# Kernel optimization log

Measured on AMD Instinct MI355X. Metric: run time of the kernel, lower is better.

Reference implementation:

```python
import jax, jax.numpy as jnp
import numpy as np

# dims: B = clips*frames, L = x spatial tokens, C = input/output/linear_out dim,
# D = conv_dim_in, NV = conv_dim_out == linear_in (visual tokens), T = num_tk
B, L, C, D, NV, T, FR = 160, 196, 768, 512, 196, 87, 10
DM, DS = C // 2, C // 16          # affine bottleneck d_model, adapter down size
ALPHA, BETA, GAMMA = 0.3, 0.05, 0.05
EPS = 1e-5


def _ln(x, g, b):
    m = x.mean(-1, keepdims=True)
    v = jnp.mean((x - m) ** 2, axis=-1, keepdims=True)
    return (x - m) * jax.lax.rsqrt(v + EPS) * g + b


def _forward(x, vis_token, conv_w, conv_b, fc_w, fc_b, my_tokens, gate_av,
             a1_w, a1_b, v1_w, v1_b, bt_w, bt_b, vc_w, vc_b, v2_w, v2_b,
             a2_w, a2_b, vs_w, vs_b, tg_w, tg_b, lnb_g, lnb_b, down_w,
             bn1_g, bn1_b, bn1_m, bn1_v, up_w, bn2_g, bn2_b, bn2_m, bn2_v,
             lnp_g, lnp_b, gate):
    vt = vis_token[..., 0]                                   # (B,NV,D)
    # conv_adapter: 1x1 conv over channel axis D -> NV, then fc over token axis NV -> C
    h = jnp.einsum('od,bnd->bon', conv_w, vt) + conv_b[None, :, None]   # (B,NV,NV)
    V = jnp.einsum('bon,cn->boc', h, fc_w) + fc_b            # (B,NV,C)  == vis_token tokens

    # token <-> visual cross-attention
    rep = jnp.broadcast_to(my_tokens, (x.shape[0], T, C))    # (B,T,C)
    att_v2tk = jax.nn.softmax(jnp.einsum('btd,bnd->btn', rep, V), axis=-1)
    rep = rep + jnp.einsum('btn,bnd->btd', att_v2tk, V)

    xt = jnp.transpose(x[..., 0], (0, 2, 1))                 # (B,L,C)
    att_tk2x = jax.nn.softmax(jnp.einsum('bld,btd->blt', xt, rep), axis=-1)
    xt = xt + gate_av * jnp.einsum('blt,btd->bld', att_tk2x, rep)

    # channel attention
    audio = V.mean(axis=1)                                   # (B,C)
    aq1 = jax.nn.relu(audio @ a1_w.T + a1_b)[:, None, :]     # (B,1,C)
    vq1 = jax.nn.relu(xt @ v1_w.T + v1_b)                    # (B,L,C)
    avq = jax.nn.relu((aq1 * vq1).mean(axis=1) @ bt_w.T + bt_b)          # (B,DM)
    ch = jax.nn.sigmoid(avq @ vc_w.T + vc_b)[:, None, :]     # (B,1,C)
    cfeat = xt * (ch + 1.0)                                  # (B,L,C)

    # spatial attention
    cq = jax.nn.relu(cfeat @ v2_w.T + v2_b)                  # (B,L,DM)
    aq2 = jax.nn.relu(audio @ a2_w.T + a2_b)[:, None, :]     # (B,1,DM)
    s_tmp = (cq * aq2) @ vs_w.T + vs_b                       # (B,L,1)
    s_sig = jax.nn.sigmoid(s_tmp)                            # (B,L,1)
    spatial = jax.nn.softmax(jnp.tanh(s_tmp).transpose(0, 2, 1), axis=-1)  # (B,1,L)

    # temporal gate over frames
    audio_r = audio.reshape(B // FR, FR, C)
    temporal = jax.nn.sigmoid(audio_r @ tg_w.T + tg_b)[..., None]          # (bs,FR,1,1)

    x5 = xt.reshape(B // FR, FR, L, C)
    factor = (ALPHA * ch.reshape(B // FR, FR, 1, C)
              + BETA * s_sig.reshape(B // FR, FR, L, 1)
              + GAMMA * temporal + (1.0 - ALPHA))
    x6 = (x5 * factor).reshape(B, L, C)

    # bottleneck adapter: LN -> down(1x1) -> BN -> ReLU -> up(1x1) -> BN -> LN -> gate
    x6 = _ln(x6, lnb_g, lnb_b)
    z = jnp.einsum('blc,oc->blo', x6, down_w)                # (B,L,DS)
    z = (z - bn1_m) * jax.lax.rsqrt(bn1_v + EPS) * bn1_g + bn1_b
    z = jax.nn.relu(z)
    o = jnp.einsum('blo,co->blc', z, up_w)                   # (B,L,C)
    o = (o - bn2_m) * jax.lax.rsqrt(bn2_v + EPS) * bn2_g + bn2_b
    o = _ln(o, lnp_g, lnp_b)
    out = (gate * o).transpose(0, 2, 1)[..., None]           # (B,C,L,1)
    return out, spatial, temporal


def setup_inputs() -> dict:
    key = jax.random.key(0)
    ks = iter(jax.random.split(key, 48))
    nrm = lambda shp, s=0.02: jax.random.normal(next(ks), shp, jnp.float32) * s
    d = {}
    d['x'] = jax.random.normal(next(ks), (B, C, L, 1), jnp.float32)
    d['vis_token'] = jax.random.normal(next(ks), (B, NV, D, 1), jnp.float32)
    d['conv_w'] = nrm((NV, D)); d['conv_b'] = jnp.zeros((NV,), jnp.float32)
    d['fc_w'] = nrm((C, NV)); d['fc_b'] = jnp.zeros((C,), jnp.float32)
    d['my_tokens'] = jax.random.uniform(next(ks), (T, C), jnp.float32)
    d['gate_av'] = jnp.float32(0.5)
    d['a1_w'] = nrm((C, C)); d['a1_b'] = jnp.zeros((C,), jnp.float32)
    d['v1_w'] = nrm((C, C)); d['v1_b'] = jnp.zeros((C,), jnp.float32)
    d['bt_w'] = nrm((DM, C)); d['bt_b'] = jnp.zeros((DM,), jnp.float32)
    d['vc_w'] = nrm((C, DM)); d['vc_b'] = jnp.zeros((C,), jnp.float32)
    d['v2_w'] = nrm((DM, C)); d['v2_b'] = jnp.zeros((DM,), jnp.float32)
    d['a2_w'] = nrm((DM, C)); d['a2_b'] = jnp.zeros((DM,), jnp.float32)
    d['vs_w'] = nrm((1, DM)); d['vs_b'] = jnp.zeros((1,), jnp.float32)
    d['tg_w'] = nrm((1, C)); d['tg_b'] = jnp.zeros((1,), jnp.float32)
    d['lnb_g'] = jnp.ones((C,), jnp.float32); d['lnb_b'] = jnp.zeros((C,), jnp.float32)
    d['down_w'] = nrm((DS, C))
    d['bn1_g'] = jnp.ones((DS,), jnp.float32); d['bn1_b'] = jnp.zeros((DS,), jnp.float32)
    d['bn1_m'] = jnp.zeros((DS,), jnp.float32); d['bn1_v'] = jnp.ones((DS,), jnp.float32)
    d['up_w'] = nrm((C, DS))
    d['bn2_g'] = jnp.ones((C,), jnp.float32); d['bn2_b'] = jnp.zeros((C,), jnp.float32)
    d['bn2_m'] = jnp.zeros((C,), jnp.float32); d['bn2_v'] = jnp.ones((C,), jnp.float32)
    d['lnp_g'] = jnp.ones((C,), jnp.float32); d['lnp_b'] = jnp.zeros((C,), jnp.float32)
    d['gate'] = jnp.float32(1.0)
    return d


def reference(x, vis_token, conv_w, conv_b, fc_w, fc_b, my_tokens, gate_av,
              a1_w, a1_b, v1_w, v1_b, bt_w, bt_b, vc_w, vc_b, v2_w, v2_b,
              a2_w, a2_b, vs_w, vs_b, tg_w, tg_b, lnb_g, lnb_b, down_w,
              bn1_g, bn1_b, bn1_m, bn1_v, up_w, bn2_g, bn2_b, bn2_m, bn2_v,
              lnp_g, lnp_b, gate):
    return _forward(x, vis_token, conv_w, conv_b, fc_w, fc_b, my_tokens, gate_av,
                    a1_w, a1_b, v1_w, v1_b, bt_w, bt_b, vc_w, vc_b, v2_w, v2_b,
                    a2_w, a2_b, vs_w, vs_b, tg_w, tg_b, lnb_g, lnb_b, down_w,
                    bn1_g, bn1_b, bn1_m, bn1_v, up_w, bn2_g, bn2_b, bn2_m, bn2_v,
                    lnp_g, lnp_b, gate)
```

## Files before the change

### kernel.cpp

```cpp
#include <hip/hip_runtime.h>
#include <math.h>

#define Bc   160
#define Lc   196
#define Cc   768
#define Dc   512
#define NVc  196
#define Tc   87
#define FRc  10
#define DMc  384
#define DSc  48
#define LROW 196
#define ALPHAc 0.3f
#define BETAc  0.05f
#define GAMMAc 0.05f
#define EPSc   1e-5f

typedef __attribute__((ext_vector_type(8))) short short8v;
typedef __attribute__((ext_vector_type(4))) short short4v;
typedef __attribute__((ext_vector_type(4))) float f32x4;

__device__ __forceinline__ short f2bf(float f) {
    unsigned u = __builtin_bit_cast(unsigned, f);
    u = (u + 0x7FFFu + ((u >> 16) & 1u)) >> 16;
    return (short)u;
}
__device__ __forceinline__ float bf2f(short s) {
    unsigned u = ((unsigned)(unsigned short)s) << 16;
    return __builtin_bit_cast(float, u);
}

__device__ __forceinline__ void gload16(const void* g, void* l) {
    using GP = const __attribute__((address_space(1))) unsigned int*;
    using LP = __attribute__((address_space(3))) unsigned int*;
    __builtin_amdgcn_global_load_lds((GP)(uintptr_t)g, (LP)(uintptr_t)l, 16, 0, 0);
}

template<int BIAS, int ACT, int OUT, int STORE, int ADDT,
         bool ASCALE, bool RSUM, bool CSCALE, bool MULP, int BMODE, bool SWZ, bool FLAT,
         bool TSTORE>
__global__ __launch_bounds__(256) void mgemm(
    const short* __restrict__ A, long sA,
    const void* __restrict__ Bp, long sB, int ldB, int Klim,
    float* __restrict__ Cf, long sCf,
    short* __restrict__ Cb, long sCb, int ldC,
    float* __restrict__ Rf, long sRf,
    const void* __restrict__ Addp, long sAdd,
    const float* __restrict__ scalePtr,
    const float* __restrict__ biasR, const float* __restrict__ biasC,
    const float* __restrict__ ascale, const float* __restrict__ wcol,
    const float* __restrict__ csc, const float* __restrict__ mulp,
    int M, int N, int K, int nI, int nJ, float outScale)
{
    constexpr bool DEEP = (BMODE == 0) && !ASCALE;
    constexpr int LDSN = DEEP ? 24576 : 16384;
    constexpr int BOFF = DEEP ? 12288 : 8192;
    __shared__ short smem[LDSN];
    int b, iT, jT;
    if (FLAT) {
        b = 0;
        int id = blockIdx.x;
        int nI8 = (nI >> 3) << 3;
        int main_ = nI8 * nJ;
        if (id < main_) { int xx = id & 7; int q = id >> 3; jT = q % nJ; iT = (q / nJ) * 8 + xx; }
        else { int id2 = id - main_; iT = nI8 + id2 / nJ; jT = id2 % nJ; }
    } else {
        const int tiles = nI * nJ;
        int t;
        if (SWZ) { int id = blockIdx.x; b = ((id >> 3) / tiles) * 8 + (id & 7); t = (id >> 3) % tiles; }
        else     { int id = blockIdx.x; b = id / tiles; t = id % tiles; }
        iT = t / nJ; jT = t % nJ;
    }
    const int i0 = iT * 128, j0 = jT * 128;
    const int tid = threadIdx.x;
    const int wl = tid & 63, w = tid >> 6;
    const int wr = (w >> 1) * 64, wc = (w & 1) * 64;
    const int lr = wl & 15;
    const int kgl = (((wl >> 4) ^ (lr & 3) ^ ((lr >> 2) & 3)) * 8);
    const int sl8 = (((tid & 3) ^ ((tid >> 2) & 3) ^ ((tid >> 4) & 3)) * 8);
    const int grow = w * 16 + (wl >> 2);
    const int srow = tid >> 2;
    const short* Ab = A + (FLAT ? 0L : (long)b * sA);

    f32x4 acc[4][4] = {};

    auto STAGE = [&](short* Asb, short* Bsb, int k0) {
        if (!ASCALE) {
            #pragma unroll
            for (int h = 0; h < 2; ++h) {
                int gi = i0 + h * 64 + grow; if (gi > M - 1) gi = M - 1;
                gload16(Ab + (long)gi * K + k0 + sl8, Asb + h * 2048 + w * 512);
            }
        } else {
            #pragma unroll
            for (int h = 0; h < 2; ++h) {
                int r = srow + h * 64;
                int gi = i0 + r; if (gi > M - 1) gi = M - 1;
                short8v av = *(const short8v*)(Ab + (long)gi * K + k0 + (tid & 3) * 8);
                int bb = FLAT ? (gi / LROW) : b;
                const float* asb = ascale + (long)bb * K + k0 + (tid & 3) * 8;
                #pragma unroll
                for (int e = 0; e < 8; ++e) av[e] = f2bf(bf2f(av[e]) * asb[e]);
                *(short8v*)&Asb[r * 32 + sl8] = av;
            }
        }
        if (BMODE == 0) {
            const short* Bb = (const short*)Bp + (FLAT ? 0L : (long)b * sB);
            #pragma unroll
            for (int h = 0; h < 2; ++h) {
                int gj = j0 + h * 64 + grow; if (gj > N - 1) gj = N - 1;
                gload16(Bb + (long)gj * K + k0 + sl8, Bsb + h * 2048 + w * 512);
            }
        } else if (BMODE == 2) {
            const float* Bb = (const float*)Bp + (long)b * sB;
            #pragma unroll
            for (int h = 0; h < 2; ++h) {
                int r = srow + h * 64;
                int gj = j0 + r;
                short8v bv = {};
                if (gj < N) {
                    const float* p = Bb + (long)gj * K + k0 + (tid & 3) * 8;
                    float4 lo = *(const float4*)p, hi = *(const float4*)(p + 4);
                    bv[0] = f2bf(lo.x); bv[1] = f2bf(lo.y); bv[2] = f2bf(lo.z); bv[3] = f2bf(lo.w);
                    bv[4] = f2bf(hi.x); bv[5] = f2bf(hi.y); bv[6] = f2bf(hi.z); bv[7] = f2bf(hi.w);
                }
                *(short8v*)&Bsb[r * 32 + sl8] = bv;
            }
        } else if (BMODE == 1) {
            const short* Bb = (const short*)Bp + (long)b * sB;
            #pragma unroll
            for (int h = 0; h < 2; ++h) {
                int idx = tid + h * 256;
                int kk = idx >> 4, jg = idx & 15;
                int gk = k0 + kk, gj = j0 + jg * 8;
                short8v bv = {};
                if (gk < Klim && gj < N)
                    bv = *(const short8v*)(Bb + (long)gk * ldB + gj);
                #pragma unroll
                for (int e = 0; e < 8; ++e) {
                    int row = jg * 8 + e;
                    int slot = (kk >> 3) ^ (row & 3) ^ ((row >> 2) & 3);
                    Bsb[row * 32 + slot * 8 + (kk & 7)] = bv[e];
                }
            }
        }
    };

    auto COMPUTE = [&](const short* as, const short* bs) {
        short8v af[4], bfv[4];
        #pragma unroll
        for (int m = 0; m < 4; ++m) af[m]  = *(const short8v*)&as[(wr + m * 16 + lr) * 32 + kgl];
        #pragma unroll
        for (int n = 0; n < 4; ++n) bfv[n] = *(const short8v*)&bs[(wc + n * 16 + lr) * 32 + kgl];
        #pragma unroll
        for (int m = 0; m < 4; ++m)
            #pragma unroll
            for (int n = 0; n < 4; ++n)
                acc[m][n] = __builtin_amdgcn_mfma_f32_16x16x32_bf16(af[m], bfv[n], acc[m][n], 0, 0, 0);
    };

    const int nt = K >> 5;
    if (DEEP) {
        STAGE(smem, smem + BOFF, 0);
        if (nt > 1) STAGE(smem + 4096, smem + BOFF + 4096, 32);
        for (int tt = 0; tt < nt; ++tt) {
            if (tt + 1 < nt) asm volatile("s_waitcnt vmcnt(4)" ::: "memory");
            else             asm volatile("s_waitcnt vmcnt(0)" ::: "memory");
            __builtin_amdgcn_s_barrier();
            __builtin_amdgcn_sched_barrier(0);
            if (tt + 2 < nt) {
                int nb = (tt + 2) % 3;
                STAGE(smem + nb * 4096, smem + BOFF + nb * 4096, (tt + 2) * 32);
            }
            int cb = tt % 3;
            COMPUTE(smem + cb * 4096, smem + BOFF + cb * 4096);
        }
    } else {
        STAGE(smem, smem + BOFF, 0);
        for (int tt = 0; tt < nt; ++tt) {
            __syncthreads();
            if (tt + 1 < nt) {
                int nb = (tt + 1) & 1;
                STAGE(smem + nb * 4096, smem + BOFF + nb * 4096, (tt + 1) * 32);
            }
            int cb = tt & 1;
            COMPUTE(smem + cb * 4096, smem + BOFF + cb * 4096);
        }
    }

    const int colbase = j0 + wc;
    const int rowbase = i0 + wr;
    float scale = 1.f;
    if (ADDT) scale = scalePtr ? scalePtr[0] : 1.f;
    const int bA = FLAT ? (i0 / LROW) : 0;
    const bool straddle = FLAT && (((i0 + 127) / LROW) != bA);

    if (OUT == 0 && TSTORE) {
        float rsum[4] = {0.f, 0.f, 0.f, 0.f};
        float rsum2[4] = {0.f, 0.f, 0.f, 0.f};
        __syncthreads();
        #pragma unroll
        for (int n = 0; n < 4; ++n) {
            int col = wc + n * 16 + lr;
            int j = j0 + col;
            int jc = j < N ? j : N - 1;
            #pragma unroll
            for (int m = 0; m < 4; ++m) {
                #pragma unroll
                for (int r = 0; r < 4; ++r) {
                    int row = wr + m * 16 + (wl >> 4) * 4 + r;
                    int i = i0 + row;
                    int ic = i < M ? i : M - 1;
                    float v = acc[m][n][r];
                    if (BIAS == 1) v += biasR[ic];
                    else if (BIAS == 2) v += biasC[jc];
                    else if (BIAS == 3) v = v * biasR[jc] + biasC[jc];
                    if (ACT == 1) v = fmaxf(v, 0.f);
                    else if (ACT == 2) v = 1.f / (1.f + expf(-v));
                    else if (ACT == 3) v = 1.f + 1.f / (1.f + expf(-v));
                    if (CSCALE) v *= csc[jc];
                    if (MULP) v *= mulp[(long)ic * N + jc];
                    smem[row * 128 + col] = f2bf(v);
                    if (RSUM && j < N && i < M) {
                        if (FLAT && (i / LROW) != bA) rsum2[n] += v;
                        else rsum[n] += v;
                    }
                }
            }
        }
        if (RSUM) {
            #pragma unroll
            for (int n = 0; n < 4; ++n) {
                int j = colbase + n * 16 + lr;
                float s = rsum[n];
                s += __shfl_xor(s, 16, 64);
                s += __shfl_xor(s, 32, 64);
                float s2 = 0.f;
                if (FLAT && straddle) {
                    s2 = rsum2[n];
                    s2 += __shfl_xor(s2, 16, 64);
                    s2 += __shfl_xor(s2, 32, 64);
                }
                if ((wl >> 4) == 0 && j < N) {
                    atomicAdd(&Rf[(long)bA * sRf + (FLAT ? 0 : (long)b * sRf) + j], s * outScale);
                    if (FLAT && straddle)
                        atomicAdd(&Rf[(long)(bA + 1) * sRf + j], s2 * outScale);
                }
            }
        }
        __syncthreads();
        #pragma unroll
        for (int p = 0; p < 8; ++p) {
            int row = (tid >> 4) + p * 16;
            int i = i0 + row;
            int c8 = (tid & 15) * 8;
            int j = j0 + c8;
            if (i < M && j < ldC) {
                short8v sv = *(const short8v*)&smem[row * 128 + c8];
                if (ADDT == 2) {
                    const short* ap = (const short*)Addp + (long)b * sAdd + (long)i * N + j;
                    short8v av = *(const short8v*)ap;
                    #pragma unroll
                    for (int e = 0; e < 8; ++e) sv[e] = f2bf(bf2f(av[e]) + scale * bf2f(sv[e]));
                } else if (ADDT == 1) {
                    const float* ap = (const float*)Addp + (long)b * sAdd + (long)i * N + j;
                    f32x4 lo = *(const f32x4*)ap, hi = *(const f32x4*)(ap + 4);
                    #pragma unroll
                    for (int e = 0; e < 4; ++e) sv[e] = f2bf(lo[e] + scale * bf2f(sv[e]));
                    #pragma unroll
                    for (int e = 0; e < 4; ++e) sv[e + 4] = f2bf(hi[e] + scale * bf2f(sv[e + 4]));
                }
                *(short8v*)&Cb[(long)b * sCb + (long)i * ldC + j] = sv;
            }
        }
    } else if (OUT == 0) {
        float rsum[4] = {0.f, 0.f, 0.f, 0.f};
        float rsum2[4] = {0.f, 0.f, 0.f, 0.f};
        #pragma unroll
        for (int n = 0; n < 4; ++n) {
            int j = colbase + n * 16 + lr;
            if (j >= N) continue;
            #pragma unroll
            for (int m = 0; m < 4; ++m) {
                #pragma unroll
                for (int r = 0; r < 4; ++r) {
                    int i = rowbase + m * 16 + (wl >> 4) * 4 + r;
                    if (i >= M) continue;
                    float v = acc[m][n][r];
                    if (BIAS == 1) v += biasR[i];
                    else if (BIAS == 2) v += biasC[j];
                    else if (BIAS == 3) v = v * biasR[j] + biasC[j];
                    if (ACT == 1) v = fmaxf(v, 0.f);
                    else if (ACT == 2) v = 1.f / (1.f + expf(-v));
                    else if (ACT == 3) v = 1.f + 1.f / (1.f + expf(-v));
                    if (CSCALE) v *= csc[j];
                    if (MULP) v *= mulp[(long)i * N + j];
                    if (ADDT == 1) v = ((const float*)Addp)[(long)b * sAdd + (long)i * N + j] + scale * v;
                    else if (ADDT == 2) v = bf2f(((const short*)Addp)[(long)b * sAdd + (long)i * N + j]) + scale * v;
                    if (STORE & 1) Cf[(long)b * sCf + (long)i * N + j] = v;
                    if (STORE & 2) Cb[(long)b * sCb + (long)i * ldC + j] = f2bf(v);
                    if (RSUM) {
                        if (FLAT && (i / LROW) != bA) rsum2[n] += v;
                        else rsum[n] += v;
                    }
                }
            }
        }
        if (RSUM) {
            #pragma unroll
            for (int n = 0; n < 4; ++n) {
                int j = colbase + n * 16 + lr;
                float s = rsum[n];
                s += __shfl_xor(s, 16, 64);
                s += __shfl_xor(s, 32, 64);
                float s2 = 0.f;
                if (FLAT && straddle) {
                    s2 = rsum2[n];
                    s2 += __shfl_xor(s2, 16, 64);
                    s2 += __shfl_xor(s2, 32, 64);
                }
                if ((wl >> 4) == 0 && j < N) {
                    atomicAdd(&Rf[(long)bA * sRf + (FLAT ? 0 : (long)b * sRf) + j], s * outScale);
                    if (FLAT && straddle)
                        atomicAdd(&Rf[(long)(bA + 1) * sRf + j], s2 * outScale);
                }
            }
        }
    } else if (OUT == 1) {
        #pragma unroll
        for (int n = 0; n < 4; ++n) {
            int j = colbase + n * 16 + lr;
            if (j < N) {
                float s = 0.f, s2 = 0.f;
                #pragma unroll
                for (int m = 0; m < 4; ++m)
                    #pragma unroll
                    for (int r = 0; r < 4; ++r) {
                        int i = rowbase + m * 16 + (wl >> 4) * 4 + r;
                        if (i >= M) continue;
                        float v = acc[m][n][r];
                        if (BIAS == 2) v += biasC[j];
                        if (ACT == 1) v = fmaxf(v, 0.f);
                        if (FLAT && (i / LROW) != bA) s2 += v; else s += v;
                    }
                s += __shfl_xor(s, 16, 64);
                s += __shfl_xor(s, 32, 64);
                if (FLAT && straddle) {
                    s2 += __shfl_xor(s2, 16, 64);
                    s2 += __shfl_xor(s2, 32, 64);
                }
                if ((wl >> 4) == 0) {
                    atomicAdd(&Cf[(long)(FLAT ? bA : b) * sCf + j], s * outScale);
                    if (FLAT && straddle)
                        atomicAdd(&Cf[(long)(bA + 1) * sCf + j], s2 * outScale);
                }
            }
        }
    } else {
        #pragma unroll
        for (int m = 0; m < 4; ++m) {
            #pragma unroll
            for (int r = 0; r < 4; ++r) {
                int i = rowbase + m * 16 + (wl >> 4) * 4 + r;
                int bw = FLAT ? (i < M ? i / LROW : 0) : b;
                float s = 0.f;
                #pragma unroll
                for (int n = 0; n < 4; ++n) {
                    int j = colbase + n * 16 + lr;
                    if (j >= N) continue;
                    float v = acc[m][n][r];
                    if (BIAS == 2) v += biasC[j];
                    if (ACT == 1) v = fmaxf(v, 0.f);
                    s += v * wcol[(long)bw * N + j];
                }
                s += __shfl_xor(s, 1, 64);
                s += __shfl_xor(s, 2, 64);
                s += __shfl_xor(s, 4, 64);
                s += __shfl_xor(s, 8, 64);
                if (lr == 0 && i < M)
                    atomicAdd(&Cf[(FLAT ? (long)i : (long)b * sCf + i)], s * outScale);
            }
        }
    }
}

__global__ void k_cvt_weights(
    const float* __restrict__ my_tok, const float* __restrict__ conv_w,
    const float* __restrict__ a1_w, const float* __restrict__ v1_w,
    const float* __restrict__ bt_w, const float* __restrict__ vc_w,
    const float* __restrict__ v2_w, const float* __restrict__ a2_w,
    const float* __restrict__ down_w, const float* __restrict__ fc_w,
    const float* __restrict__ up_w,
    short* __restrict__ mytok_bf, short* __restrict__ wconv,
    short* __restrict__ wa1, short* __restrict__ wv1,
    short* __restrict__ wbt, short* __restrict__ wvc,
    short* __restrict__ wv2, short* __restrict__ wa2,
    short* __restrict__ wdown, short* __restrict__ wfc, short* __restrict__ wup)
{
    long idx = (long)blockIdx.x * 256 + threadIdx.x;
    if (idx < 66816)  { mytok_bf[idx] = f2bf(my_tok[idx]); return; }  idx -= 66816;
    if (idx < 100352) { wconv[idx] = f2bf(conv_w[idx]); return; }     idx -= 100352;
    if (idx < 589824) { wa1[idx] = f2bf(a1_w[idx]); return; }         idx -= 589824;
    if (idx < 589824) { wv1[idx] = f2bf(v1_w[idx]); return; }         idx -= 589824;
    if (idx < 294912) { wbt[idx] = f2bf(bt_w[idx]); return; }         idx -= 294912;
    if (idx < 294912) { wvc[idx] = f2bf(vc_w[idx]); return; }         idx -= 294912;
    if (idx < 294912) { wv2[idx] = f2bf(v2_w[idx]); return; }         idx -= 294912;
    if (idx < 294912) { wa2[idx] = f2bf(a2_w[idx]); return; }         idx -= 294912;
    if (idx < 36864)  { wdown[idx] = f2bf(down_w[idx]); return; }     idx -= 36864;
    if (idx < 172032) { int r = (int)(idx / 224), c = (int)(idx % 224);
                        wfc[idx] = (c < 196) ? f2bf(fc_w[(long)r * 196 + c]) : (short)0; return; }
    idx -= 172032;
    if (idx < 49152)  { int r = (int)(idx / 64), c = (int)(idx % 64);
                        wup[idx] = (c < 48) ? f2bf(up_w[(long)r * 48 + c]) : (short)0; }
}

__global__ void k_prep(const float* g1, const float* b1, const float* m1, const float* v1,
                       const float* g2, const float* b2, const float* m2, const float* v2,
                       float* scl1, float* sft1, float* scl2, float* sft2)
{
    int j = threadIdx.x;
    if (j < DSc) { float r = rsqrtf(v1[j] + EPSc) * g1[j]; scl1[j] = r; sft1[j] = b1[j] - m1[j] * r; }
    if (j < Cc)  { float r = rsqrtf(v2[j] + EPSc) * g2[j]; scl2[j] = r; sft2[j] = b2[j] - m2[j] * r; }
}

__global__ __launch_bounds__(256) void k_transpose(const float* __restrict__ x, short* __restrict__ xtb)
{
    __shared__ float tile[64][33];
    int b = blockIdx.z;
    int c0 = blockIdx.y * 64, l0 = blockIdx.x * 32;
    int tx = threadIdx.x & 31, ty = threadIdx.x >> 5;
    #pragma unroll
    for (int k = 0; k < 8; ++k) {
        int c = c0 + ty + 8 * k, l = l0 + tx;
        tile[ty + 8 * k][tx] = (l < Lc) ? x[((long)b * Cc + c) * Lc + l] : 0.f;
    }
    __syncthreads();
    int cg = threadIdx.x & 15, lw = threadIdx.x >> 4;
    #pragma unroll
    for (int p = 0; p < 2; ++p) {
        int l = l0 + lw + p * 16;
        if (l >= Lc) continue;
        int c = c0 + cg * 4;
        short4v sv;
        #pragma unroll
        for (int e = 0; e < 4; ++e) sv[e] = f2bf(tile[cg * 4 + e][lw + p * 16]);
        *(short4v*)(xtb + ((long)b * Lc + l) * Cc + c) = sv;
    }
}

__global__ __launch_bounds__(256) void k_audio_fin(
    const float* __restrict__ audio, short* __restrict__ audio_bf,
    const float* __restrict__ tg_w, const float* __restrict__ tg_b,
    float* __restrict__ tempv, float* __restrict__ outTemp)
{
    __shared__ float red[256];
    int b = blockIdx.x, tid = threadIdx.x;
    float part = 0.f;
    #pragma unroll
    for (int q = 0; q < 3; ++q) {
        int c = tid + q * 256;
        float a = audio[(long)b * Cc + c];
        audio_bf[(long)b * Cc + c] = f2bf(a);
        part += a * tg_w[c];
    }
    red[tid] = part; __syncthreads();
    for (int s = 128; s > 0; s >>= 1) { if (tid < s) red[tid] += red[tid + s]; __syncthreads(); }
    if (tid == 0) {
        float t = 1.f / (1.f + expf(-(red[0] + tg_b[0])));
        tempv[b] = t; outTemp[b] = t;
    }
}

__global__ __launch_bounds__(256) void k_softmax_w(const float* __restrict__ in,
                                                   short* __restrict__ out,
                                                   int n, int ldo, int rows)
{
    int r = blockIdx.x * 4 + (threadIdx.x >> 6);
    int lane = threadIdx.x & 63;
    if (r >= rows) return;
    const float* row = in + (long)r * n;
    float v[4];
    float mx = -INFINITY;
    #pragma unroll
    for (int q = 0; q < 4; ++q) {
        int c = lane + q * 64;
        v[q] = (c < n) ? row[c] : -INFINITY;
        mx = fmaxf(mx, v[q]);
    }
    #pragma unroll
    for (int off = 32; off > 0; off >>= 1) mx = fmaxf(mx, __shfl_xor(mx, off, 64));
    float sum = 0.f;
    #pragma unroll
    for (int q = 0; q < 4; ++q) {
        int c = lane + q * 64;
        float e = (c < n) ? expf(v[q] - mx) : 0.f;
        v[q] = e; sum += e;
    }
    #pragma unroll
    for (int off = 32; off > 0; off >>= 1) sum += __shfl_xor(sum, off, 64);
    float inv = 1.0f / sum;
    #pragma unroll
    for (int q = 0; q < 4; ++q) {
        int c = lane + q * 64;
        if (c < ldo) out[(long)r * ldo + c] = (c < n) ? f2bf(v[q] * inv) : (short)0;
    }
}

__global__ __launch_bounds__(256) void k_spatial(const float* __restrict__ stmp,
                                                 const float* __restrict__ vs_b,
                                                 float* __restrict__ ssig,
                                                 float* __restrict__ spat)
{
    __shared__ float red[256];
    int b = blockIdx.x, tid = threadIdx.x;
    float t = -INFINITY;
    if (tid < Lc) {
        float v = stmp[(long)b * Lc + tid] + vs_b[0];
        ssig[(long)b * Lc + tid] = 1.f / (1.f + expf(-v));
        t = tanhf(v);
    }
    red[tid] = t; __syncthreads();
    for (int s = 128; s > 0; s >>= 1) { if (tid < s) red[tid] = fmaxf(red[tid], red[tid + s]); __syncthreads(); }
    float mx = red[0]; __syncthreads();
    float e = (tid < Lc) ? expf(t - mx) : 0.f;
    red[tid] = e; __syncthreads();
    for (int s = 128; s > 0; s >>= 1) { if (tid < s) red[tid] += red[tid + s]; __syncthreads(); }
    if (tid < Lc) spat[(long)b * Lc + tid] = e / red[0];
}

__global__ __launch_bounds__(256) void k_ln_factor(
    short* __restrict__ xt, const float* __restrict__ chp1,
    const float* __restrict__ ssig, const float* __restrict__ tmp_,
    const float* __restrict__ g, const float* __restrict__ be)
{
    long r = (long)blockIdx.x * 4 + (threadIdx.x >> 6);
    int lane = threadIdx.x & 63;
    int b = (int)(r / Lc);
    float rowterm = BETAc * ssig[r] + GAMMAc * tmp_[b] + (1.0f - ALPHAc);
    float v[12];
    #pragma unroll
    for (int q = 0; q < 3; ++q) {
        int c = lane * 4 + q * 256;
        short4v sv = *(const short4v*)(xt + r * Cc + c);
        f32x4 ch = *(const f32x4*)(chp1 + (long)b * Cc + c);
        #pragma unroll
        for (int e = 0; e < 4; ++e)
            v[q * 4 + e] = bf2f(sv[e]) * (ALPHAc * (ch[e] - 1.0f) + rowterm);
    }
    float s = 0.f;
    #pragma unroll
    for (int e = 0; e < 12; ++e) s += v[e];
    #pragma unroll
    for (int off = 32; off > 0; off >>= 1) s += __shfl_xor(s, off, 64);
    float mean = s * (1.0f / Cc);
    float var = 0.f;
    #pragma unroll
    for (int e = 0; e < 12; ++e) { float d = v[e] - mean; var += d * d; }
    #pragma unroll
    for (int off = 32; off > 0; off >>= 1) var += __shfl_xor(var, off, 64);
    float rs = rsqrtf(var * (1.0f / Cc) + EPSc);
    #pragma unroll
    for (int q = 0; q < 3; ++q) {
        int c = lane * 4 + q * 256;
        f32x4 gv = *(const f32x4*)(g + c);
        f32x4 bv = *(const f32x4*)(be + c);
        short4v sv;
        #pragma unroll
        for (int e = 0; e < 4; ++e)
            sv[e] = f2bf((v[q * 4 + e] - mean) * rs * gv[e] + bv[e]);
        *(short4v*)(xt + r * Cc + c) = sv;
    }
}

__global__ __launch_bounds__(256) void k_final(
    const short* __restrict__ o,
    const float* __restrict__ lng, const float* __restrict__ lnb,
    const float* __restrict__ gatePtr, float* __restrict__ out)
{
    __shared__ short ot[16 * 776];
    __shared__ float mean_s[16], rsv_s[16];
    int lt = blockIdx.x, b = blockIdx.y;
    int l0 = lt * 16;
    int tid = threadIdx.x;
    int rows = Lc - l0; if (rows > 16) rows = 16;
    const short* src = o + ((long)b * Lc + l0) * Cc;
    int n8 = rows * 96;
    for (int idx = tid; idx < n8; idx += 256) {
        int rr = idx / 96, c8 = idx % 96;
        short8v val = *(const short8v*)(src + (long)rr * Cc + c8 * 8);
        *(short8v*)&ot[rr * 776 + c8 * 8] = val;
    }
    __syncthreads();
    int w = tid >> 6, lane = tid & 63;
    for (int rr = w; rr < rows; rr += 4) {
        float v[12];
        #pragma unroll
        for (int q = 0; q < 3; ++q) {
            int c = lane * 4 + q * 256;
            short4v sv = *(const short4v*)&ot[rr * 776 + c];
            #pragma unroll
            for (int e = 0; e < 4; ++e) v[q * 4 + e] = bf2f(sv[e]);
        }
        float s = 0.f;
        #pragma unroll
        for (int e = 0; e < 12; ++e) s += v[e];
        #pragma unroll
        for (int off = 32; off > 0; off >>= 1) s += __shfl_xor(s, off, 64);
        float mean = s * (1.0f / Cc);
        float var = 0.f;
        #pragma unroll
        for (int e = 0; e < 12; ++e) { float d = v[e] - mean; var += d * d; }
        #pragma unroll
        for (int off = 32; off > 0; off >>= 1) var += __shfl_xor(var, off, 64);
        if (lane == 0) {
            mean_s[rr] = mean;
            rsv_s[rr] = rsqrtf(var * (1.0f / Cc) + EPSc);
        }
    }
    __syncthreads();
    float gate = gatePtr[0];
    if (rows == 16) {
        for (int idx = tid; idx < Cc * 4; idx += 256) {
            int c = idx >> 2, q = idx & 3;
            float lg = lng[c], lb = lnb[c];
            f32x4 val;
            #pragma unroll
            for (int e = 0; e < 4; ++e) {
                int rr = q * 4 + e;
                float xv = bf2f(ot[rr * 776 + c]);
                val[e] = gate * ((xv - mean_s[rr]) * rsv_s[rr] * lg + lb);
            }
            *(f32x4*)(out + ((long)b * Cc + c) * Lc + l0 + q * 4) = val;
        }
    } else {
        for (int idx = tid; idx < Cc; idx += 256) {
            int c = idx;
            float lg = lng[c], lb = lnb[c];
            f32x4 val;
            #pragma unroll
            for (int e = 0; e < 4; ++e) {
                float xv = bf2f(ot[e * 776 + c]);
                val[e] = gate * ((xv - mean_s[e]) * rsv_s[e] * lg + lb);
            }
            *(f32x4*)(out + ((long)b * Cc + c) * Lc + l0) = val;
        }
    }
}

extern "C" void kernel_launch(void* const* d_in, const int* in_sizes, int n_in,
                              void* d_out, int out_size, void* d_ws, size_t ws_size,
                              hipStream_t stream)
{
    const float* x       = (const float*)d_in[0];
    const float* vis     = (const float*)d_in[1];
    const float* conv_w  = (const float*)d_in[2];
    const float* conv_b  = (const float*)d_in[3];
    const float* fc_w    = (const float*)d_in[4];
    const float* fc_b    = (const float*)d_in[5];
    const float* my_tok  = (const float*)d_in[6];
    const float* gate_av = (const float*)d_in[7];
    const float* a1_w    = (const float*)d_in[8];
    const float* a1_b    = (const float*)d_in[9];
    const float* v1_w    = (const float*)d_in[10];
    const float* v1_b    = (const float*)d_in[11];
    const float* bt_w    = (const float*)d_in[12];
    const float* bt_b    = (const float*)d_in[13];
    const float* vc_w    = (const float*)d_in[14];
    const float* vc_b    = (const float*)d_in[15];
    const float* v2_w    = (const float*)d_in[16];
    const float* v2_b    = (const float*)d_in[17];
    const float* a2_w    = (const float*)d_in[18];
    const float* a2_b    = (const float*)d_in[19];
    const float* vs_w    = (const float*)d_in[20];
    const float* vs_b    = (const float*)d_in[21];
    const float* tg_w    = (const float*)d_in[22];
    const float* tg_b    = (const float*)d_in[23];
    const float* lnb_g   = (const float*)d_in[24];
    const float* lnb_b   = (const float*)d_in[25];
    const float* down_w  = (const float*)d_in[26];
    const float* bn1_g   = (const float*)d_in[27];
    const float* bn1_b   = (const float*)d_in[28];
    const float* bn1_m   = (const float*)d_in[29];
    const float* bn1_v   = (const float*)d_in[30];
    const float* up_w    = (const float*)d_in[31];
    const float* bn2_g   = (const float*)d_in[32];
    const float* bn2_b   = (const float*)d_in[33];
    const float* bn2_m   = (const float*)d_in[34];
    const float* bn2_v   = (const float*)d_in[35];
    const float* lnp_g   = (const float*)d_in[36];
    const float* lnp_b   = (const float*)d_in[37];
    const float* gate    = (const float*)d_in[38];

    float* out = (float*)d_out;
    float* outSpat = out + (long)Bc * Cc * Lc;
    float* outTemp = outSpat + (long)Bc * Lc;

    float* wsf   = (float*)d_ws;
    float* scoresf = wsf;
    float* audio = scoresf + 2729280L;
    float* vq1m  = audio + 122880L;
    float* stmp  = vq1m + 122880L;
    float* chp1  = stmp + 31360L;
    float* aq2   = chp1 + 122880L;
    float* ssig  = aq2 + 61440L;
    float* tempv = ssig + 31360L;
    float* bnscl1 = tempv + 192L;
    float* bnsft1 = bnscl1 + 64L;
    float* bnscl2 = bnsft1 + 64L;
    float* bnsft2 = bnscl2 + 768L;
    short* wss   = (short*)(bnsft2 + 768L);
    short* P2    = wss;
    short* P3    = P2 + 24084480L;
    short* P4    = P3 + 10690560L;
    short* zb_bf = P4 + 3118080L;
    short* audio_bf = zb_bf + 2007040L;
    short* avqin_bf = audio_bf + 122880L;
    short* avq_bf   = avqin_bf + 122880L;
    short* mytok_bf = avq_bf + 61440L;
    short* wconv = mytok_bf + 66816L;
    short* wa1   = wconv + 100352L;
    short* wv1   = wa1 + 589824L;
    short* wbt   = wv1 + 589824L;
    short* wvc   = wbt + 294912L;
    short* wv2   = wvc + 294912L;
    short* wa2   = wv2 + 294912L;
    short* wdown = wa2 + 294912L;
    short* wfc   = wdown + 36864L;
    short* wup   = wfc + 172032L;

    dim3 blk(256);
    auto cgrid = [](long n) { return dim3((unsigned)((n + 255) / 256)); };
    const int MF = Bc * Lc;

    k_cvt_weights<<<cgrid(2784512L), blk, 0, stream>>>(
        my_tok, conv_w, a1_w, v1_w, bt_w, vc_w, v2_w, a2_w, down_w, fc_w, up_w,
        mytok_bf, wconv, wa1, wv1, wbt, wvc, wv2, wa2, wdown, wfc, wup);
    k_prep<<<1, 768, 0, stream>>>(bn1_g, bn1_b, bn1_m, bn1_v,
                                  bn2_g, bn2_b, bn2_m, bn2_v,
                                  bnscl1, bnsft1, bnscl2, bnsft2);
    hipMemsetAsync(audio, 0, (size_t)(122880 + 122880 + 31360) * sizeof(float), stream);

    mgemm<1,0,0,2,0,false,false,false,false,2,true,false,true><<<dim3(160*4), blk, 0, stream>>>(
        wconv, 0, vis, (long)NVc*Dc, 0, Dc, nullptr, 0, P3, (long)NVc*224, 224,
        nullptr, 0, nullptr, 0, nullptr, conv_b, nullptr, nullptr, nullptr, nullptr, nullptr,
        NVc, NVc, Dc, 2, 2, 1.f);

    mgemm<2,0,0,2,0,false,true,false,false,0,false,true,true><<<dim3(245*6), blk, 0, stream>>>(
        P3, 0, wfc, 0, 0, 224, nullptr, 0, P2, 0, Cc,
        audio, Cc, nullptr, 0, nullptr, nullptr, fc_b, nullptr, nullptr, nullptr, nullptr,
        MF, Cc, 224, 245, 6, 1.0f/NVc);

    k_audio_fin<<<dim3(Bc), blk, 0, stream>>>(audio, audio_bf, tg_w, tg_b, tempv, outTemp);

    mgemm<0,0,0,1,0,false,false,false,false,0,true,false,false><<<dim3(160*2), blk, 0, stream>>>(
        mytok_bf, 0, P2, (long)NVc*Cc, 0, Cc, scoresf, (long)Tc*NVc, nullptr, 0, 0,
        nullptr, 0, nullptr, 0, nullptr, nullptr, nullptr, nullptr, nullptr, nullptr, nullptr,
        Tc, NVc, Cc, 1, 2, 1.f);

    k_softmax_w<<<dim3((Bc*Tc+3)/4), blk, 0, stream>>>(scoresf, P4, NVc, 224, Bc*Tc);

    mgemm<0,0,0,2,1,false,false,false,false,1,true,false,true><<<dim3(160*6), blk, 0, stream>>>(
        P4, (long)Tc*224, P2, (long)NVc*Cc, Cc, NVc, nullptr, 0, P3, (long)Tc*Cc, Cc,
        nullptr, 0, my_tok, 0, nullptr, nullptr, nullptr, nullptr, nullptr, nullptr, nullptr,
        Tc, Cc, 224, 1, 6, 1.f);

    k_transpose<<<dim3(7,12,Bc), blk, 0, stream>>>(x, P2);

    mgemm<0,0,0,1,0,false,false,false,false,0,true,false,false><<<dim3(160*2), blk, 0, stream>>>(
        P2, (long)Lc*Cc, P3, (long)Tc*Cc, 0, Cc, scoresf, (long)Lc*Tc, nullptr, 0, 0,
        nullptr, 0, nullptr, 0, nullptr, nullptr, nullptr, nullptr, nullptr, nullptr, nullptr,
        Lc, Tc, Cc, 2, 1, 1.f);

    k_softmax_w<<<dim3((Bc*Lc+3)/4), blk, 0, stream>>>(scoresf, P4, Tc, 96, Bc*Lc);

    mgemm<0,0,0,2,2,false,false,false,false,1,true,false,true><<<dim3(160*12), blk, 0, stream>>>(
        P4, (long)Lc*96, P3, (long)Tc*Cc, Cc, Tc, nullptr, 0, P2, (long)Lc*Cc, Cc,
        nullptr, 0, P2, (long)Lc*Cc, gate_av, nullptr, nullptr, nullptr, nullptr, nullptr, nullptr,
        Lc, Cc, 96, 2, 6, 1.f);

    mgemm<2,1,1,0,0,false,false,false,false,0,false,true,false><<<dim3(245*6), blk, 0, stream>>>(
        P2, 0, wv1, 0, 0, Cc, vq1m, Cc, nullptr, 0, 0,
        nullptr, 0, nullptr, 0, nullptr, nullptr, v1_b, nullptr, nullptr, nullptr, nullptr,
        MF, Cc, Cc, 245, 6, 1.0f/Lc);

    mgemm<2,1,0,2,0,false,false,false,true,0,false,false,true><<<dim3(12), blk, 0, stream>>>(
        audio_bf, 0, wa1, 0, 0, Cc, nullptr, 0, avqin_bf, 0, Cc,
        nullptr, 0, nullptr, 0, nullptr, nullptr, a1_b, nullptr, nullptr, nullptr, vq1m,
        Bc, Cc, Cc, 2, 6, 1.f);

    mgemm<2,1,0,2,0,false,false,false,false,0,false,false,true><<<dim3(6), blk, 0, stream>>>(
        avqin_bf, 0, wbt, 0, 0, Cc, nullptr, 0, avq_bf, 0, DMc,
        nullptr, 0, nullptr, 0, nullptr, nullptr, bt_b, nullptr, nullptr, nullptr, nullptr,
        Bc, DMc, Cc, 2, 3, 1.f);

    mgemm<2,3,0,1,0,false,false,false,false,0,false,false,false><<<dim3(12), blk, 0, stream>>>(
        avq_bf, 0, wvc, 0, 0, DMc, chp1, 0, nullptr, 0, 0,
        nullptr, 0, nullptr, 0, nullptr, nullptr, vc_b, nullptr, nullptr, nullptr, nullptr,
        Bc, Cc, DMc, 2, 6, 1.f);

    mgemm<2,1,0,1,0,false,false,true,false,0,false,false,false><<<dim3(6), blk, 0, stream>>>(
        audio_bf, 0, wa2, 0, 0, Cc, aq2, 0, nullptr, 0, 0,
        nullptr, 0, nullptr, 0, nullptr, nullptr, a2_b, nullptr, nullptr, vs_w, nullptr,
        Bc, DMc, Cc, 2, 3, 1.f);

    mgemm<2,1,2,0,0,true,false,false,false,0,false,true,false><<<dim3(245*3), blk, 0, stream>>>(
        P2, 0, wv2, 0, 0, Cc, stmp, 0, nullptr, 0, 0,
        nullptr, 0, nullptr, 0, nullptr, nullptr, v2_b, chp1, aq2, nullptr, nullptr,
        MF, DMc, Cc, 245, 3, 1.f);

    k_spatial<<<dim3(Bc), blk, 0, stream>>>(stmp, vs_b, ssig, outSpat);

    k_ln_factor<<<dim3(Bc*Lc/4), blk, 0, stream>>>(
        P2, chp1, ssig, tempv, lnb_g, lnb_b);

    mgemm<3,1,0,2,0,false,false,false,false,0,false,true,true><<<dim3(245), blk, 0, stream>>>(
        P2, 0, wdown, 0, 0, Cc, nullptr, 0, zb_bf, 0, 64,
        nullptr, 0, nullptr, 0, nullptr, bnscl1, bnsft1, nullptr, nullptr, nullptr, nullptr,
        MF, DSc, Cc, 245, 1, 1.f);

    mgemm<3,0,0,2,0,false,false,false,false,0,false,true,true><<<dim3(245*6), blk, 0, stream>>>(
        zb_bf, 0, wup, 0, 0, 64, nullptr, 0, P2, 0, Cc,
        nullptr, 0, nullptr, 0, nullptr, bnscl2, bnsft2, nullptr, nullptr, nullptr, nullptr,
        MF, Cc, 64, 245, 6, 1.f);

    k_final<<<dim3(13,Bc), blk, 0, stream>>>(
        P2, lnp_g, lnp_b, gate, out);
}
```

Baseline: 550.4 us.

## Prefetch register-staged GEMM operands one tile ahead and pre-convert vis tokens to bf16

In the non-deep GEMM path, the tile loads that pass through registers (scaled A, transposed B, fp32 B) are split into a global-load step and an LDS-write step. Loads for tile k+2 are issued before computing tile k, so global latency overlaps MFMA work. The conv GEMM's fp32 vis-token operand is also converted to bf16 by a new separate kernel, which lets that GEMM use the async direct-to-LDS load path instead of converting inside the loop. The cost is extra register pressure and an additional pass that reads the vis tensor and writes a bf16 copy of it.

```diff
diff --git a/kernel.cpp b/kernel.cpp
--- a/kernel.cpp
+++ b/kernel.cpp
@@ -84,66 +84,112 @@
 
     f32x4 acc[4][4] = {};
 
-    auto STAGE = [&](short* Asb, short* Bsb, int k0) {
-        if (!ASCALE) {
-            #pragma unroll
-            for (int h = 0; h < 2; ++h) {
-                int gi = i0 + h * 64 + grow; if (gi > M - 1) gi = M - 1;
-                gload16(Ab + (long)gi * K + k0 + sl8, Asb + h * 2048 + w * 512);
-            }
-        } else {
-            #pragma unroll
-            for (int h = 0; h < 2; ++h) {
-                int r = srow + h * 64;
-                int gi = i0 + r; if (gi > M - 1) gi = M - 1;
-                short8v av = *(const short8v*)(Ab + (long)gi * K + k0 + (tid & 3) * 8);
-                int bb = FLAT ? (gi / LROW) : b;
-                const float* asb = ascale + (long)bb * K + k0 + (tid & 3) * 8;
-                #pragma unroll
-                for (int e = 0; e < 8; ++e) av[e] = f2bf(bf2f(av[e]) * asb[e]);
-                *(short8v*)&Asb[r * 32 + sl8] = av;
-            }
-        }
-        if (BMODE == 0) {
-            const short* Bb = (const short*)Bp + (FLAT ? 0L : (long)b * sB);
-            #pragma unroll
-            for (int h = 0; h < 2; ++h) {
-                int gj = j0 + h * 64 + grow; if (gj > N - 1) gj = N - 1;
-                gload16(Bb + (long)gj * K + k0 + sl8, Bsb + h * 2048 + w * 512);
-            }
-        } else if (BMODE == 2) {
-            const float* Bb = (const float*)Bp + (long)b * sB;
-            #pragma unroll
-            for (int h = 0; h < 2; ++h) {
-                int r = srow + h * 64;
-                int gj = j0 + r;
-                short8v bv = {};
-                if (gj < N) {
-                    const float* p = Bb + (long)gj * K + k0 + (tid & 3) * 8;
-                    float4 lo = *(const float4*)p, hi = *(const float4*)(p + 4);
-                    bv[0] = f2bf(lo.x); bv[1] = f2bf(lo.y); bv[2] = f2bf(lo.z); bv[3] = f2bf(lo.w);
-                    bv[4] = f2bf(hi.x); bv[5] = f2bf(hi.y); bv[6] = f2bf(hi.z); bv[7] = f2bf(hi.w);
-                }
-                *(short8v*)&Bsb[r * 32 + sl8] = bv;
-            }
-        } else if (BMODE == 1) {
-            const short* Bb = (const short*)Bp + (long)b * sB;
-            #pragma unroll
-            for (int h = 0; h < 2; ++h) {
-                int idx = tid + h * 256;
-                int kk = idx >> 4, jg = idx & 15;
-                int gk = k0 + kk, gj = j0 + jg * 8;
-                short8v bv = {};
-                if (gk < Klim && gj < N)
-                    bv = *(const short8v*)(Bb + (long)gk * ldB + gj);
-                #pragma unroll
-                for (int e = 0; e < 8; ++e) {
-                    int row = jg * 8 + e;
-                    int slot = (kk >> 3) ^ (row & 3) ^ ((row >> 2) & 3);
-                    Bsb[row * 32 + slot * 8 + (kk & 7)] = bv[e];
-                }
-            }
-        }
+    auto GLA = [&](short* Asb, int k0) {
+        #pragma unroll
+        for (int h = 0; h < 2; ++h) {
+            int gi = i0 + h * 64 + grow; if (gi > M - 1) gi = M - 1;
+            gload16(Ab + (long)gi * K + k0 + sl8, Asb + h * 2048 + w * 512);
+        }
+    };
+    auto GLB = [&](short* Bsb, int k0) {
+        const short* Bb = (const short*)Bp + (FLAT ? 0L : (long)b * sB);
+        #pragma unroll
+        for (int h = 0; h < 2; ++h) {
+            int gj = j0 + h * 64 + grow; if (gj > N - 1) gj = N - 1;
+            gload16(Bb + (long)gj * K + k0 + sl8, Bsb + h * 2048 + w * 512);
+        }
+    };
+    auto LDA_R = [&](int k0, short8v& a0, short8v& a1) {
+        {
+            int gi = i0 + srow; if (gi > M - 1) gi = M - 1;
+            short8v av = *(const short8v*)(Ab + (long)gi * K + k0 + (tid & 3) * 8);
+            int bb = FLAT ? (gi / LROW) : b;
+            const float* asb = ascale + (long)bb * K + k0 + (tid & 3) * 8;
+            #pragma unroll
+            for (int e = 0; e < 8; ++e) av[e] = f2bf(bf2f(av[e]) * asb[e]);
+            a0 = av;
+        }
+        {
+            int gi = i0 + srow + 64; if (gi > M - 1) gi = M - 1;
+            short8v av = *(const short8v*)(Ab + (long)gi * K + k0 + (tid & 3) * 8);
+            int bb = FLAT ? (gi / LROW) : b;
+            const float* asb = ascale + (long)bb * K + k0 + (tid & 3) * 8;
+            #pragma unroll
+            for (int e = 0; e < 8; ++e) av[e] = f2bf(bf2f(av[e]) * asb[e]);
+            a1 = av;
+        }
+    };
+    auto WRA_R = [&](short* Asb, short8v a0, short8v a1) {
+        *(short8v*)&Asb[srow * 32 + sl8] = a0;
+        *(short8v*)&Asb[(srow + 64) * 32 + sl8] = a1;
+    };
+    auto LDB1_R = [&](int k0, short8v& b0, short8v& b1) {
+        const short* Bb = (const short*)Bp + (long)b * sB;
+        {
+            int kk = tid >> 4, jg = tid & 15;
+            int gk = k0 + kk, gj = j0 + jg * 8;
+            short8v bv = {};
+            if (gk < Klim && gj < N) bv = *(const short8v*)(Bb + (long)gk * ldB + gj);
+            b0 = bv;
+        }
+        {
+            int idx = tid + 256;
+            int kk = idx >> 4, jg = idx & 15;
+            int gk = k0 + kk, gj = j0 + jg * 8;
+            short8v bv = {};
+            if (gk < Klim && gj < N) bv = *(const short8v*)(Bb + (long)gk * ldB + gj);
+            b1 = bv;
+        }
+    };
+    auto WRB1_R = [&](short* Bsb, short8v b0, short8v b1) {
+        {
+            int kk = tid >> 4, jg = tid & 15;
+            #pragma unroll
+            for (int e = 0; e < 8; ++e) {
+                int row = jg * 8 + e;
+                int slot = (kk >> 3) ^ (row & 3) ^ ((row >> 2) & 3);
+                Bsb[row * 32 + slot * 8 + (kk & 7)] = b0[e];
+            }
+        }
+        {
+            int idx = tid + 256;
+            int kk = idx >> 4, jg = idx & 15;
+            #pragma unroll
+            for (int e = 0; e < 8; ++e) {
+                int row = jg * 8 + e;
+                int slot = (kk >> 3) ^ (row & 3) ^ ((row >> 2) & 3);
+                Bsb[row * 32 + slot * 8 + (kk & 7)] = b1[e];
+            }
+        }
+    };
+    auto LDB2_R = [&](int k0, short8v& b0, short8v& b1) {
+        const float* Bb = (const float*)Bp + (long)b * sB;
+        {
+            int gj = j0 + srow;
+            short8v bv = {};
+            if (gj < N) {
+                const float* p = Bb + (long)gj * K + k0 + (tid & 3) * 8;
+                float4 lo = *(const float4*)p, hi = *(const float4*)(p + 4);
+                bv[0] = f2bf(lo.x); bv[1] = f2bf(lo.y); bv[2] = f2bf(lo.z); bv[3] = f2bf(lo.w);
+                bv[4] = f2bf(hi.x); bv[5] = f2bf(hi.y); bv[6] = f2bf(hi.z); bv[7] = f2bf(hi.w);
+            }
+            b0 = bv;
+        }
+        {
+            int gj = j0 + srow + 64;
+            short8v bv = {};
+            if (gj < N) {
+                const float* p = Bb + (long)gj * K + k0 + (tid & 3) * 8;
+                float4 lo = *(const float4*)p, hi = *(const float4*)(p + 4);
+                bv[0] = f2bf(lo.x); bv[1] = f2bf(lo.y); bv[2] = f2bf(lo.z); bv[3] = f2bf(lo.w);
+                bv[4] = f2bf(hi.x); bv[5] = f2bf(hi.y); bv[6] = f2bf(hi.z); bv[7] = f2bf(hi.w);
+            }
+            b1 = bv;
+        }
+    };
+    auto WRB2_R = [&](short* Bsb, short8v b0, short8v b1) {
+        *(short8v*)&Bsb[srow * 32 + sl8] = b0;
+        *(short8v*)&Bsb[(srow + 64) * 32 + sl8] = b1;
     };
 
     auto COMPUTE = [&](const short* as, const short* bs) {
@@ -161,8 +207,8 @@
 
     const int nt = K >> 5;
     if (DEEP) {
-        STAGE(smem, smem + BOFF, 0);
-        if (nt > 1) STAGE(smem + 4096, smem + BOFF + 4096, 32);
+        GLA(smem, 0); GLB(smem + BOFF, 0);
+        if (nt > 1) { GLA(smem + 4096, 32); GLB(smem + BOFF + 4096, 32); }
         for (int tt = 0; tt < nt; ++tt) {
             if (tt + 1 < nt) asm volatile("s_waitcnt vmcnt(4)" ::: "memory");
             else             asm volatile("s_waitcnt vmcnt(0)" ::: "memory");
@@ -170,21 +216,42 @@
             __builtin_amdgcn_sched_barrier(0);
             if (tt + 2 < nt) {
                 int nb = (tt + 2) % 3;
-                STAGE(smem + nb * 4096, smem + BOFF + nb * 4096, (tt + 2) * 32);
+                GLA(smem + nb * 4096, (tt + 2) * 32);
+                GLB(smem + BOFF + nb * 4096, (tt + 2) * 32);
             }
             int cb = tt % 3;
             COMPUTE(smem + cb * 4096, smem + BOFF + cb * 4096);
         }
     } else {
-        STAGE(smem, smem + BOFF, 0);
+        short8v rA0{}, rA1{}, rB0{}, rB1{};
+        if (ASCALE) { LDA_R(0, rA0, rA1); WRA_R(smem, rA0, rA1); }
+        else GLA(smem, 0);
+        if (BMODE == 1) { LDB1_R(0, rB0, rB1); WRB1_R(smem + BOFF, rB0, rB1); }
+        else if (BMODE == 2) { LDB2_R(0, rB0, rB1); WRB2_R(smem + BOFF, rB0, rB1); }
+        else GLB(smem + BOFF, 0);
+        if (nt > 1) {
+            if (ASCALE) LDA_R(32, rA0, rA1);
+            if (BMODE == 1) LDB1_R(32, rB0, rB1);
+            else if (BMODE == 2) LDB2_R(32, rB0, rB1);
+        }
         for (int tt = 0; tt < nt; ++tt) {
             __syncthreads();
             if (tt + 1 < nt) {
-                int nb = (tt + 1) & 1;
-                STAGE(smem + nb * 4096, smem + BOFF + nb * 4096, (tt + 1) * 32);
-            }
-            int cb = tt & 1;
-            COMPUTE(smem + cb * 4096, smem + BOFF + cb * 4096);
+                short* ab  = smem + ((tt + 1) & 1) * 4096;
+                short* bb2 = smem + BOFF + ((tt + 1) & 1) * 4096;
+                if (ASCALE) WRA_R(ab, rA0, rA1); else GLA(ab, (tt + 1) * 32);
+                if (BMODE == 1) WRB1_R(bb2, rB0, rB1);
+                else if (BMODE == 2) WRB2_R(bb2, rB0, rB1);
+                else GLB(bb2, (tt + 1) * 32);
+            }
+            short8v nA0 = rA0, nA1 = rA1, nB0 = rB0, nB1 = rB1;
+            if (tt + 2 < nt) {
+                if (ASCALE) LDA_R((tt + 2) * 32, nA0, nA1);
+                if (BMODE == 1) LDB1_R((tt + 2) * 32, nB0, nB1);
+                else if (BMODE == 2) LDB2_R((tt + 2) * 32, nB0, nB1);
+            }
+            COMPUTE(smem + (tt & 1) * 4096, smem + BOFF + (tt & 1) * 4096);
+            rA0 = nA0; rA1 = nA1; rB0 = nB0; rB1 = nB1;
         }
     }
 
@@ -382,6 +449,18 @@
             }
         }
     }
+}
+
+__global__ __launch_bounds__(256) void k_cvt_vis(const float* __restrict__ in,
+                                                 short* __restrict__ out, long n)
+{
+    long i = ((long)blockIdx.x * 256 + threadIdx.x) * 8;
+    if (i >= n) return;
+    f32x4 lo = *(const f32x4*)(in + i), hi = *(const f32x4*)(in + i + 4);
+    short8v s;
+    s[0] = f2bf(lo[0]); s[1] = f2bf(lo[1]); s[2] = f2bf(lo[2]); s[3] = f2bf(lo[3]);
+    s[4] = f2bf(hi[0]); s[5] = f2bf(hi[1]); s[6] = f2bf(hi[2]); s[7] = f2bf(hi[3]);
+    *(short8v*)(out + i) = s;
 }
 
 __global__ void k_cvt_weights(
@@ -727,11 +806,13 @@
     short* wdown = wa2 + 294912L;
     short* wfc   = wdown + 36864L;
     short* wup   = wfc + 172032L;
+    short* vtbf  = wup + 49152L;
 
     dim3 blk(256);
     auto cgrid = [](long n) { return dim3((unsigned)((n + 255) / 256)); };
     const int MF = Bc * Lc;
 
+    k_cvt_vis<<<dim3(7840), blk, 0, stream>>>(vis, vtbf, 16056320L);
     k_cvt_weights<<<cgrid(2784512L), blk, 0, stream>>>(
         my_tok, conv_w, a1_w, v1_w, bt_w, vc_w, v2_w, a2_w, down_w, fc_w, up_w,
         mytok_bf, wconv, wa1, wv1, wbt, wvc, wv2, wa2, wdown, wfc, wup);
@@ -740,8 +821,8 @@
                                   bnscl1, bnsft1, bnscl2, bnsft2);
     hipMemsetAsync(audio, 0, (size_t)(122880 + 122880 + 31360) * sizeof(float), stream);
 
-    mgemm<1,0,0,2,0,false,false,false,false,2,true,false,true><<<dim3(160*4), blk, 0, stream>>>(
-        wconv, 0, vis, (long)NVc*Dc, 0, Dc, nullptr, 0, P3, (long)NVc*224, 224,
+    mgemm<1,0,0,2,0,false,false,false,false,0,true,false,true><<<dim3(160*4), blk, 0, stream>>>(
+        wconv, 0, vtbf, (long)NVc*Dc, 0, 0, nullptr, 0, P3, (long)NVc*224, 224,
         nullptr, 0, nullptr, 0, nullptr, conv_b, nullptr, nullptr, nullptr, nullptr, nullptr,
         NVc, NVc, Dc, 2, 2, 1.f);
 
```

Result: faster. 533.4 us (-3.1%).
